# Kernel tuning notes

Hardware: AMD Instinct MI355X
Metric: run time of the kernel (lower is better)

## Reference

```python
import jax, jax.numpy as jnp
import numpy as np

B, N, C = 2, 4096, 768
H = 12  # num_heads; head_dim = C // H = 64


def setup_inputs() -> dict:
    key = jax.random.key(0)
    kx, kq, kk, kv = jax.random.split(key, 4)
    s = C ** -0.5  # keep param magnitudes sane
    return {
        "x": jax.random.normal(kx, (B, N, C), dtype=jnp.float32),
        "Wq": jax.random.normal(kq, (C, C), dtype=jnp.float32) * s,
        "Wk": jax.random.normal(kk, (C, C), dtype=jnp.float32) * s,
        "Wv": jax.random.normal(kv, (C, C), dtype=jnp.float32) * s,  # created but UNUSED, as in original
    }


def reference(x, Wq, Wk, Wv):
    b, n, c = x.shape
    hd = c // H
    # torch nn.Linear: y = x @ W.T
    q = (x @ Wq.T).reshape(b, n, H, hd).transpose(0, 2, 1, 3)  # [B,H,N,hd]
    k = (x @ Wk.T).reshape(b, n, H, hd).transpose(0, 2, 1, 3)
    # BUG preserved from source: value path uses the K projection, Wv is unused
    v = (x @ Wk.T).reshape(b, n, H, hd).transpose(0, 2, 1, 3)
    # scale by full C (not head_dim), as in source
    attn = jnp.einsum("bhqd,bhkd->bhqk", q, k) * (c ** -0.5)
    attn = jax.nn.softmax(attn, axis=-1)
    out = jnp.einsum("bhqk,bhkd->bhqd", attn, v)  # [B,H,N,hd]
    return out.transpose(0, 2, 1, 3).reshape(b, n, c)
```

## Files before the change

kernel.cpp:

```cpp
#include <hip/hip_runtime.h>

typedef __bf16 bf16;
typedef __bf16 bf16x4 __attribute__((ext_vector_type(4)));
typedef __bf16 bf16x8 __attribute__((ext_vector_type(8)));
typedef float  f32x4  __attribute__((ext_vector_type(4)));
typedef int    int4v  __attribute__((ext_vector_type(4)));

#define NTOK 4096
#define NH   12
#define HD   64
#define CDIM 768

#define K2SCALE 0.05205928442089389f

__device__ __forceinline__ bf16* swz(bf16* base, int row, int byteoff) {
  return (bf16*)((char*)base + row * 128 +
                 ((((byteoff >> 4) ^ (row & 7)) << 4) | (byteoff & 15)));
}
__device__ __forceinline__ const bf16* swz(const bf16* base, int row, int byteoff) {
  return (const bf16*)((const char*)base + row * 128 +
                 ((((byteoff >> 4) ^ (row & 7)) << 4) | (byteoff & 15)));
}

__global__ __launch_bounds__(256) void cast_kernel(
    const float* __restrict__ x, const float* __restrict__ wq, const float* __restrict__ wk,
    bf16* __restrict__ xb, bf16* __restrict__ wqb, bf16* __restrict__ wkb,
    long nx, long nw) {
  long i4 = ((long)blockIdx.x * 256 + threadIdx.x) * 4;
  if (i4 >= nx + 2 * nw) return;
  const float* src; bf16* dst;
  if (i4 < nx)            { src = x  + i4;            dst = xb  + i4; }
  else if (i4 < nx + nw)  { src = wq + (i4 - nx);     dst = wqb + (i4 - nx); }
  else                    { src = wk + (i4 - nx - nw); dst = wkb + (i4 - nx - nw); }
  f32x4 v = *(const f32x4*)src;
  *(bf16x4*)dst = __builtin_convertvector(v, bf16x4);
}

__global__ __launch_bounds__(256) void proj_kernel(
    const bf16* __restrict__ xb, const bf16* __restrict__ wqb, const bf16* __restrict__ wkb,
    bf16* __restrict__ Qb, bf16* __restrict__ Kb) {
  __shared__ __align__(16) bf16 Ap[128 * 64];
  __shared__ __align__(16) bf16 Bp[128 * 64];
  const int tid = threadIdx.x;
  const int w = tid >> 6, lane = tid & 63, l15 = lane & 15, quad = lane >> 4;
  const int m0 = blockIdx.x * 128;
  const int j0 = blockIdx.y * 128;
  const bf16* W   = blockIdx.z ? wkb : wqb;
  bf16*       Out = blockIdx.z ? Kb  : Qb;
  const float oscale = blockIdx.z ? 1.0f : K2SCALE;

  const int srow = tid >> 3, scb = (tid & 7) * 16, soff = (tid & 7) * 8;
  const bf16* pa = xb + (long)(m0 + srow) * CDIM + soff;
  const bf16* pb = W  + (long)(j0 + srow) * CDIM + soff;

  f32x4 acc[2][8] = {};
  int4v rA[4], rB[4];
#pragma unroll
  for (int i = 0; i < 4; ++i) {
    rA[i] = *(const int4v*)(pa + (long)i * 32 * CDIM);
    rB[i] = *(const int4v*)(pb + (long)i * 32 * CDIM);
  }

  for (int kt = 0; kt < CDIM / 64; ++kt) {
    __syncthreads();
#pragma unroll
    for (int i = 0; i < 4; ++i) {
      *(int4v*)swz(Ap, srow + i * 32, scb) = rA[i];
      *(int4v*)swz(Bp, srow + i * 32, scb) = rB[i];
    }
    __syncthreads();
    const long koff = (long)((kt == CDIM / 64 - 1) ? kt : kt + 1) * 64;
#pragma unroll
    for (int i = 0; i < 4; ++i) {
      rA[i] = *(const int4v*)(pa + (long)i * 32 * CDIM + koff);
      rB[i] = *(const int4v*)(pb + (long)i * 32 * CDIM + koff);
    }
#pragma unroll
    for (int kk = 0; kk < 2; ++kk) {
      bf16x8 a[2], b[8];
#pragma unroll
      for (int rt = 0; rt < 2; ++rt)
        a[rt] = *(const bf16x8*)swz(Ap, w * 32 + rt * 16 + l15, kk * 64 + quad * 16);
#pragma unroll
      for (int ct = 0; ct < 8; ++ct)
        b[ct] = *(const bf16x8*)swz(Bp, ct * 16 + l15, kk * 64 + quad * 16);
#pragma unroll
      for (int rt = 0; rt < 2; ++rt)
#pragma unroll
        for (int ct = 0; ct < 8; ++ct)
          acc[rt][ct] = __builtin_amdgcn_mfma_f32_16x16x32_bf16(a[rt], b[ct], acc[rt][ct], 0, 0, 0);
    }
  }
#pragma unroll
  for (int rt = 0; rt < 2; ++rt)
#pragma unroll
    for (int ct = 0; ct < 8; ++ct)
#pragma unroll
      for (int reg = 0; reg < 4; ++reg) {
        int m = m0 + w * 32 + rt * 16 + quad * 4 + reg;
        int j = j0 + ct * 16 + l15;
        int b = m >> 12, n = m & (NTOK - 1);
        int h = j >> 6, d = j & (HD - 1);
        Out[(((long)(b * NH + h) * NTOK + n) << 6) + d] = (bf16)(acc[rt][ct][reg] * oscale);
      }
}

__global__ __launch_bounds__(256) void transpose_kernel(
    const bf16* __restrict__ Kb, bf16* __restrict__ Ktb) {
  __shared__ __align__(16) bf16 T[64 * 72];
  const int tid = threadIdx.x;
  const int n0 = blockIdx.x * 64;
  const long bh = blockIdx.y;
#pragma unroll
  for (int i = 0; i < 2; ++i) {
    int c = tid + i * 256;
    int row = c >> 3, off = (c & 7) * 8;
    bf16x8 v = *(const bf16x8*)(Kb + ((bh << 12) + n0 + row) * HD + off);
#pragma unroll
    for (int e = 0; e < 8; ++e) T[(off + e) * 72 + row] = v[e];
  }
  __syncthreads();
#pragma unroll
  for (int i = 0; i < 2; ++i) {
    int c = tid + i * 256;
    int d = c >> 3, koff = (c & 7) * 8;
    int4v v = *(const int4v*)(&T[d * 72 + koff]);
    *(int4v*)(Ktb + ((bh << 6) + d) * (long)NTOK + n0 + koff) = v;
  }
}

__global__ __launch_bounds__(256) void attn_kernel(
    const bf16* __restrict__ Qb, const bf16* __restrict__ Kb, const bf16* __restrict__ Ktb,
    float* __restrict__ out) {
  __shared__ __align__(16) bf16 QP[128 * 64];
  __shared__ __align__(16) bf16 Ks[64 * 64];
  __shared__ __align__(16) bf16 Kts[64 * 64];

  const int tid = threadIdx.x;
  const int w = tid >> 6, lane = tid & 63, l15 = lane & 15, quad = lane >> 4;
  const int q0 = blockIdx.x * 128;
  const int bh = blockIdx.y;
  const int b = bh / NH, h = bh % NH;
  const bf16* Qhead  = Qb  + (long)bh * NTOK * HD;
  const bf16* Khead  = Kb  + (long)bh * NTOK * HD;
  const bf16* Kthead = Ktb + (long)bh * HD * NTOK;

  const int srow = tid >> 3, scb = (tid & 7) * 16, soff = (tid & 7) * 8;
  const bf16* pk  = Khead  + (long)srow * HD + soff;
  const bf16* pkt = Kthead + (long)srow * NTOK + soff;

#pragma unroll
  for (int i = 0; i < 4; ++i) {
    int c = tid + i * 256;
    int row = c >> 3, cb = (c & 7) * 16;
    int4v v = *(const int4v*)(Qhead + (long)(q0 + row) * HD + (c & 7) * 8);
    *(int4v*)swz(QP, row, cb) = v;
  }

  int4v rK[2], rKt[2];
#pragma unroll
  for (int i = 0; i < 2; ++i) {
    rK[i]  = *(const int4v*)(pk  + (long)i * 32 * HD);
    rKt[i] = *(const int4v*)(pkt + (long)i * 32 * NTOK);
  }

  __syncthreads();
  bf16x8 bq[2][2];
#pragma unroll
  for (int nt = 0; nt < 2; ++nt)
#pragma unroll
    for (int kk = 0; kk < 2; ++kk)
      bq[nt][kk] = *(const bf16x8*)swz(QP, w * 32 + nt * 16 + l15, kk * 64 + quad * 16);

  f32x4 o[4][2] = {};
  float lacc[2] = {0.f, 0.f};

  for (int kt = 0; kt < NTOK / 64; ++kt) {
    __syncthreads();
#pragma unroll
    for (int i = 0; i < 2; ++i) {
      *(int4v*)swz(Ks,  srow + i * 32, scb) = rK[i];
      *(int4v*)swz(Kts, srow + i * 32, scb) = rKt[i];
    }
    __syncthreads();

    const long knext = (long)((kt == NTOK / 64 - 1) ? kt : kt + 1) * 64;
#pragma unroll
    for (int i = 0; i < 2; ++i) {
      rK[i]  = *(const int4v*)(pk  + knext * HD + (long)i * 32 * HD);
      rKt[i] = *(const int4v*)(pkt + knext + (long)i * 32 * NTOK);
    }

    f32x4 s[4][2] = {};
#pragma unroll
    for (int kk = 0; kk < 2; ++kk) {
      bf16x8 ak[4];
#pragma unroll
      for (int mt = 0; mt < 4; ++mt)
        ak[mt] = *(const bf16x8*)swz(Ks, mt * 16 + l15, kk * 64 + quad * 16);
#pragma unroll
      for (int mt = 0; mt < 4; ++mt)
#pragma unroll
        for (int nt = 0; nt < 2; ++nt)
          s[mt][nt] = __builtin_amdgcn_mfma_f32_16x16x32_bf16(ak[mt], bq[nt][kk], s[mt][nt], 0, 0, 0);
    }

#pragma unroll
    for (int mt = 0; mt < 4; ++mt)
#pragma unroll
      for (int nt = 0; nt < 2; ++nt) {
        f32x4 p;
#pragma unroll
        for (int reg = 0; reg < 4; ++reg) p[reg] = __builtin_amdgcn_exp2f(s[mt][nt][reg]);
        lacc[nt] += (p[0] + p[1]) + (p[2] + p[3]);
        *(bf16x4*)swz(QP, w * 32 + nt * 16 + l15, mt * 32 + quad * 8) =
            __builtin_convertvector(p, bf16x4);
      }

#pragma unroll
    for (int kk = 0; kk < 2; ++kk) {
      bf16x8 av[4], bp[2];
#pragma unroll
      for (int mt = 0; mt < 4; ++mt)
        av[mt] = *(const bf16x8*)swz(Kts, mt * 16 + l15, kk * 64 + quad * 16);
#pragma unroll
      for (int nt = 0; nt < 2; ++nt)
        bp[nt] = *(const bf16x8*)swz(QP, w * 32 + nt * 16 + l15, kk * 64 + quad * 16);
#pragma unroll
      for (int mt = 0; mt < 4; ++mt)
#pragma unroll
        for (int nt = 0; nt < 2; ++nt)
          o[mt][nt] = __builtin_amdgcn_mfma_f32_16x16x32_bf16(av[mt], bp[nt], o[mt][nt], 0, 0, 0);
    }
  }

#pragma unroll
  for (int nt = 0; nt < 2; ++nt) {
    float l = lacc[nt];
    l += __shfl_xor(l, 16, 64);
    l += __shfl_xor(l, 32, 64);
    float rl = 1.0f / l;
    int n = q0 + w * 32 + nt * 16 + l15;
#pragma unroll
    for (int mt = 0; mt < 4; ++mt) {
      f32x4 v;
#pragma unroll
      for (int reg = 0; reg < 4; ++reg) v[reg] = o[mt][nt][reg] * rl;
      *(f32x4*)(&out[((long)(b * NTOK + n)) * CDIM + h * HD + mt * 16 + quad * 4]) = v;
    }
  }
}

extern "C" void kernel_launch(void* const* d_in, const int* in_sizes, int n_in,
                              void* d_out, int out_size, void* d_ws, size_t ws_size,
                              hipStream_t stream) {
  const float* x  = (const float*)d_in[0];
  const float* Wq = (const float*)d_in[1];
  const float* Wk = (const float*)d_in[2];
  float* out = (float*)d_out;
  char* ws = (char*)d_ws;

  const long NX = (long)2 * NTOK * CDIM;
  const long NW = (long)CDIM * CDIM;

  bf16* xb  = (bf16*)(ws);
  bf16* Ktb = (bf16*)(ws);
  bf16* wqb = (bf16*)(ws + NX * 2);
  bf16* wkb = (bf16*)(ws + NX * 2 + NW * 2);
  bf16* Qb  = (bf16*)(ws + NX * 2 + NW * 4);
  bf16* Kb  = (bf16*)(ws + NX * 2 + NW * 4 + NX * 2);

  long tot4 = (NX + 2 * NW) / 4;
  cast_kernel<<<dim3((tot4 + 255) / 256), 256, 0, stream>>>(x, Wq, Wk, xb, wqb, wkb, NX, NW);
  proj_kernel<<<dim3(8192 / 128, CDIM / 128, 2), 256, 0, stream>>>(xb, wqb, wkb, Qb, Kb);
  transpose_kernel<<<dim3(NTOK / 64, 2 * NH), 256, 0, stream>>>(Kb, Ktb);
  attn_kernel<<<dim3(NTOK / 128, 2 * NH), 256, 0, stream>>>(Qb, Kb, Ktb, out);
}
```

Measured before the change: 237.2 us.

## Split attention key range across two blocks and add combine kernel

Adds a grid z-dimension that splits the key loop into halves, with each block writing unnormalized partial outputs and row sums to workspace. A new combine kernel sums the partials and normalizes into the final output. This raises parallelism and shortens each block's serial loop, at the cost of extra global traffic for the partial buffers and one more launch. It falls back to the single-pass path when the workspace is too small.

```diff
diff --git a/kernel.cpp b/kernel.cpp
--- a/kernel.cpp
+++ b/kernel.cpp
@@ -131,7 +131,8 @@
 
 __global__ __launch_bounds__(256) void attn_kernel(
     const bf16* __restrict__ Qb, const bf16* __restrict__ Kb, const bf16* __restrict__ Ktb,
-    float* __restrict__ out) {
+    float* __restrict__ out, float* __restrict__ Opart, float* __restrict__ lpart,
+    int nsplit) {
   __shared__ __align__(16) bf16 QP[128 * 64];
   __shared__ __align__(16) bf16 Ks[64 * 64];
   __shared__ __align__(16) bf16 Kts[64 * 64];
@@ -140,7 +141,10 @@
   const int w = tid >> 6, lane = tid & 63, l15 = lane & 15, quad = lane >> 4;
   const int q0 = blockIdx.x * 128;
   const int bh = blockIdx.y;
+  const int half = blockIdx.z;
   const int b = bh / NH, h = bh % NH;
+  const int ktiles = (NTOK / 64) / nsplit;
+  const int kt0 = half * ktiles, kt1 = kt0 + ktiles;
   const bf16* Qhead  = Qb  + (long)bh * NTOK * HD;
   const bf16* Khead  = Kb  + (long)bh * NTOK * HD;
   const bf16* Kthead = Ktb + (long)bh * HD * NTOK;
@@ -160,8 +164,8 @@
   int4v rK[2], rKt[2];
 #pragma unroll
   for (int i = 0; i < 2; ++i) {
-    rK[i]  = *(const int4v*)(pk  + (long)i * 32 * HD);
-    rKt[i] = *(const int4v*)(pkt + (long)i * 32 * NTOK);
+    rK[i]  = *(const int4v*)(pk  + (long)kt0 * 64 * HD + (long)i * 32 * HD);
+    rKt[i] = *(const int4v*)(pkt + (long)kt0 * 64 + (long)i * 32 * NTOK);
   }
 
   __syncthreads();
@@ -175,7 +179,7 @@
   f32x4 o[4][2] = {};
   float lacc[2] = {0.f, 0.f};
 
-  for (int kt = 0; kt < NTOK / 64; ++kt) {
+  for (int kt = kt0; kt < kt1; ++kt) {
     __syncthreads();
 #pragma unroll
     for (int i = 0; i < 2; ++i) {
@@ -184,7 +188,7 @@
     }
     __syncthreads();
 
-    const long knext = (long)((kt == NTOK / 64 - 1) ? kt : kt + 1) * 64;
+    const long knext = (long)((kt == kt1 - 1) ? kt : kt + 1) * 64;
 #pragma unroll
     for (int i = 0; i < 2; ++i) {
       rK[i]  = *(const int4v*)(pk  + knext * HD + (long)i * 32 * HD);
@@ -234,21 +238,55 @@
     }
   }
 
-#pragma unroll
-  for (int nt = 0; nt < 2; ++nt) {
-    float l = lacc[nt];
-    l += __shfl_xor(l, 16, 64);
-    l += __shfl_xor(l, 32, 64);
-    float rl = 1.0f / l;
-    int n = q0 + w * 32 + nt * 16 + l15;
-#pragma unroll
-    for (int mt = 0; mt < 4; ++mt) {
-      f32x4 v;
-#pragma unroll
-      for (int reg = 0; reg < 4; ++reg) v[reg] = o[mt][nt][reg] * rl;
-      *(f32x4*)(&out[((long)(b * NTOK + n)) * CDIM + h * HD + mt * 16 + quad * 4]) = v;
-    }
-  }
+  if (nsplit == 1) {
+#pragma unroll
+    for (int nt = 0; nt < 2; ++nt) {
+      float l = lacc[nt];
+      l += __shfl_xor(l, 16, 64);
+      l += __shfl_xor(l, 32, 64);
+      float rl = 1.0f / l;
+      int n = q0 + w * 32 + nt * 16 + l15;
+#pragma unroll
+      for (int mt = 0; mt < 4; ++mt) {
+        f32x4 v;
+#pragma unroll
+        for (int reg = 0; reg < 4; ++reg) v[reg] = o[mt][nt][reg] * rl;
+        *(f32x4*)(&out[((long)(b * NTOK + n)) * CDIM + h * HD + mt * 16 + quad * 4]) = v;
+      }
+    }
+  } else {
+    const long rbase = ((long)(half * 2 * NH + bh)) << 12;
+#pragma unroll
+    for (int nt = 0; nt < 2; ++nt) {
+      float l = lacc[nt];
+      l += __shfl_xor(l, 16, 64);
+      l += __shfl_xor(l, 32, 64);
+      int n = q0 + w * 32 + nt * 16 + l15;
+      if (quad == 0) lpart[rbase + n] = l;
+#pragma unroll
+      for (int mt = 0; mt < 4; ++mt)
+        *(f32x4*)(&Opart[((rbase + n) << 6) + mt * 16 + quad * 4]) = o[mt][nt];
+    }
+  }
+}
+
+__global__ __launch_bounds__(256) void combine_kernel(
+    const float* __restrict__ Opart, const float* __restrict__ lpart,
+    float* __restrict__ out) {
+  const int t = threadIdx.x;
+  const long r = (long)blockIdx.x * 16 + (t >> 4);
+  const int d = (t & 15) * 4;
+  const long RS = (long)2 * NH * NTOK;
+  f32x4 a = *(const f32x4*)(Opart + (r << 6) + d);
+  f32x4 c = *(const f32x4*)(Opart + ((RS + r) << 6) + d);
+  float l = lpart[r] + lpart[RS + r];
+  float rl = 1.0f / l;
+  int bh = (int)(r >> 12), n = (int)(r & (NTOK - 1));
+  int b = bh / NH, h = bh % NH;
+  f32x4 v;
+#pragma unroll
+  for (int e = 0; e < 4; ++e) v[e] = (a[e] + c[e]) * rl;
+  *(f32x4*)(&out[((long)(b * NTOK + n)) * CDIM + h * HD + d]) = v;
 }
 
 extern "C" void kernel_launch(void* const* d_in, const int* in_sizes, int n_in,
@@ -269,10 +307,20 @@
   bf16* wkb = (bf16*)(ws + NX * 2 + NW * 2);
   bf16* Qb  = (bf16*)(ws + NX * 2 + NW * 4);
   bf16* Kb  = (bf16*)(ws + NX * 2 + NW * 4 + NX * 2);
+  const size_t base = (size_t)(NX * 6 + NW * 4);
+
+  const long ROWS = (long)2 * NH * NTOK;
+  float* Opart = (float*)(ws + base);
+  float* lpart = (float*)(ws + base + (size_t)2 * ROWS * HD * 4);
+  const size_t need = base + (size_t)2 * ROWS * HD * 4 + (size_t)2 * ROWS * 4;
+  const int nsplit = (ws_size >= need) ? 2 : 1;
 
   long tot4 = (NX + 2 * NW) / 4;
   cast_kernel<<<dim3((tot4 + 255) / 256), 256, 0, stream>>>(x, Wq, Wk, xb, wqb, wkb, NX, NW);
   proj_kernel<<<dim3(8192 / 128, CDIM / 128, 2), 256, 0, stream>>>(xb, wqb, wkb, Qb, Kb);
   transpose_kernel<<<dim3(NTOK / 64, 2 * NH), 256, 0, stream>>>(Kb, Ktb);
-  attn_kernel<<<dim3(NTOK / 128, 2 * NH), 256, 0, stream>>>(Qb, Kb, Ktb, out);
-}
+  attn_kernel<<<dim3(NTOK / 128, 2 * NH, nsplit), 256, 0, stream>>>(
+      Qb, Kb, Ktb, out, Opart, lpart, nsplit);
+  if (nsplit == 2)
+    combine_kernel<<<dim3(ROWS / 16), 256, 0, stream>>>(Opart, lpart, out);
+}
```

New measurement: 252.6 us. 1.06x slower.

## Split attention warps 2x2 over query and key halves with LDS reduction

Applied to the files above, without the earlier changes.

Reassigns the four waves of the attention block from a 4-way query split into a 2x2 split over query halves (64 rows) and key halves (32 keys) of each tile. Each wave now loads fewer K fragments per QK^T step and does a single PV k-step, which cuts redundant LDS reads of K and Kt. The cost is a larger output accumulator per wave (4x4 tiles instead of 4x2, more registers) and an end-of-kernel cross-wave reduction of partial outputs and row sums through shared memory.

```diff
diff --git a/kernel.cpp b/kernel.cpp
--- a/kernel.cpp
+++ b/kernel.cpp
@@ -132,12 +132,15 @@
 __global__ __launch_bounds__(256) void attn_kernel(
     const bf16* __restrict__ Qb, const bf16* __restrict__ Kb, const bf16* __restrict__ Ktb,
     float* __restrict__ out) {
-  __shared__ __align__(16) bf16 QP[128 * 64];
-  __shared__ __align__(16) bf16 Ks[64 * 64];
-  __shared__ __align__(16) bf16 Kts[64 * 64];
+  __shared__ __align__(16) bf16 SH[128 * 64 + 64 * 64 + 64 * 64 + 1024];
+  bf16* QP  = SH;
+  bf16* Ks  = SH + 128 * 64;
+  bf16* Kts = SH + 128 * 64 + 64 * 64;
+  float* lbuf = (float*)(SH + 128 * 64 + 2 * 64 * 64);
 
   const int tid = threadIdx.x;
   const int w = tid >> 6, lane = tid & 63, l15 = lane & 15, quad = lane >> 4;
+  const int qhalf = w >> 1, khalf = w & 1;
   const int q0 = blockIdx.x * 128;
   const int bh = blockIdx.y;
   const int b = bh / NH, h = bh % NH;
@@ -165,15 +168,15 @@
   }
 
   __syncthreads();
-  bf16x8 bq[2][2];
-#pragma unroll
-  for (int nt = 0; nt < 2; ++nt)
+  bf16x8 bq[4][2];
+#pragma unroll
+  for (int nt = 0; nt < 4; ++nt)
 #pragma unroll
     for (int kk = 0; kk < 2; ++kk)
-      bq[nt][kk] = *(const bf16x8*)swz(QP, w * 32 + nt * 16 + l15, kk * 64 + quad * 16);
-
-  f32x4 o[4][2] = {};
-  float lacc[2] = {0.f, 0.f};
+      bq[nt][kk] = *(const bf16x8*)swz(QP, qhalf * 64 + nt * 16 + l15, kk * 64 + quad * 16);
+
+  f32x4 o[4][4] = {};
+  float lacc[4] = {0.f, 0.f, 0.f, 0.f};
 
   for (int kt = 0; kt < NTOK / 64; ++kt) {
     __syncthreads();
@@ -191,62 +194,82 @@
       rKt[i] = *(const int4v*)(pkt + knext + (long)i * 32 * NTOK);
     }
 
-    f32x4 s[4][2] = {};
+    f32x4 s[2][4] = {};
 #pragma unroll
     for (int kk = 0; kk < 2; ++kk) {
-      bf16x8 ak[4];
-#pragma unroll
-      for (int mt = 0; mt < 4; ++mt)
-        ak[mt] = *(const bf16x8*)swz(Ks, mt * 16 + l15, kk * 64 + quad * 16);
-#pragma unroll
-      for (int mt = 0; mt < 4; ++mt)
-#pragma unroll
-        for (int nt = 0; nt < 2; ++nt)
+      bf16x8 ak[2];
+#pragma unroll
+      for (int mt = 0; mt < 2; ++mt)
+        ak[mt] = *(const bf16x8*)swz(Ks, khalf * 32 + mt * 16 + l15, kk * 64 + quad * 16);
+#pragma unroll
+      for (int mt = 0; mt < 2; ++mt)
+#pragma unroll
+        for (int nt = 0; nt < 4; ++nt)
           s[mt][nt] = __builtin_amdgcn_mfma_f32_16x16x32_bf16(ak[mt], bq[nt][kk], s[mt][nt], 0, 0, 0);
     }
 
 #pragma unroll
-    for (int mt = 0; mt < 4; ++mt)
-#pragma unroll
-      for (int nt = 0; nt < 2; ++nt) {
+    for (int mt = 0; mt < 2; ++mt)
+#pragma unroll
+      for (int nt = 0; nt < 4; ++nt) {
         f32x4 p;
 #pragma unroll
         for (int reg = 0; reg < 4; ++reg) p[reg] = __builtin_amdgcn_exp2f(s[mt][nt][reg]);
         lacc[nt] += (p[0] + p[1]) + (p[2] + p[3]);
-        *(bf16x4*)swz(QP, w * 32 + nt * 16 + l15, mt * 32 + quad * 8) =
+        *(bf16x4*)swz(QP, qhalf * 64 + nt * 16 + l15, khalf * 64 + mt * 32 + quad * 8) =
             __builtin_convertvector(p, bf16x4);
       }
 
-#pragma unroll
-    for (int kk = 0; kk < 2; ++kk) {
-      bf16x8 av[4], bp[2];
-#pragma unroll
-      for (int mt = 0; mt < 4; ++mt)
-        av[mt] = *(const bf16x8*)swz(Kts, mt * 16 + l15, kk * 64 + quad * 16);
-#pragma unroll
-      for (int nt = 0; nt < 2; ++nt)
-        bp[nt] = *(const bf16x8*)swz(QP, w * 32 + nt * 16 + l15, kk * 64 + quad * 16);
-#pragma unroll
-      for (int mt = 0; mt < 4; ++mt)
-#pragma unroll
-        for (int nt = 0; nt < 2; ++nt)
-          o[mt][nt] = __builtin_amdgcn_mfma_f32_16x16x32_bf16(av[mt], bp[nt], o[mt][nt], 0, 0, 0);
-    }
-  }
-
-#pragma unroll
-  for (int nt = 0; nt < 2; ++nt) {
+    bf16x8 av[4], bp[4];
+#pragma unroll
+    for (int mt = 0; mt < 4; ++mt)
+      av[mt] = *(const bf16x8*)swz(Kts, mt * 16 + l15, khalf * 64 + quad * 16);
+#pragma unroll
+    for (int nt = 0; nt < 4; ++nt)
+      bp[nt] = *(const bf16x8*)swz(QP, qhalf * 64 + nt * 16 + l15, khalf * 64 + quad * 16);
+#pragma unroll
+    for (int mt = 0; mt < 4; ++mt)
+#pragma unroll
+      for (int nt = 0; nt < 4; ++nt)
+        o[mt][nt] = __builtin_amdgcn_mfma_f32_16x16x32_bf16(av[mt], bp[nt], o[mt][nt], 0, 0, 0);
+  }
+
+  float lq[4];
+#pragma unroll
+  for (int nt = 0; nt < 4; ++nt) {
     float l = lacc[nt];
     l += __shfl_xor(l, 16, 64);
     l += __shfl_xor(l, 32, 64);
-    float rl = 1.0f / l;
-    int n = q0 + w * 32 + nt * 16 + l15;
-#pragma unroll
-    for (int mt = 0; mt < 4; ++mt) {
-      f32x4 v;
-#pragma unroll
-      for (int reg = 0; reg < 4; ++reg) v[reg] = o[mt][nt][reg] * rl;
-      *(f32x4*)(&out[((long)(b * NTOK + n)) * CDIM + h * HD + mt * 16 + quad * 4]) = v;
+    lq[nt] = l;
+  }
+  __syncthreads();
+  float* sc = qhalf ? (float*)Ks : (float*)QP;
+  if (khalf == 1) {
+#pragma unroll
+    for (int mt = 0; mt < 4; ++mt)
+#pragma unroll
+      for (int nt = 0; nt < 4; ++nt)
+        *(f32x4*)(sc + ((mt * 4 + nt) * 64 + lane) * 4) = o[mt][nt];
+#pragma unroll
+    for (int nt = 0; nt < 4; ++nt) lbuf[qhalf * 256 + nt * 64 + lane] = lq[nt];
+  }
+  __syncthreads();
+  if (khalf == 0) {
+    float rl[4];
+#pragma unroll
+    for (int nt = 0; nt < 4; ++nt)
+      rl[nt] = 1.0f / (lq[nt] + lbuf[qhalf * 256 + nt * 64 + lane]);
+#pragma unroll
+    for (int nt = 0; nt < 4; ++nt) {
+      int n = q0 + qhalf * 64 + nt * 16 + l15;
+#pragma unroll
+      for (int mt = 0; mt < 4; ++mt) {
+        f32x4 po = *(const f32x4*)(sc + ((mt * 4 + nt) * 64 + lane) * 4);
+        f32x4 v;
+#pragma unroll
+        for (int reg = 0; reg < 4; ++reg) v[reg] = (o[mt][nt][reg] + po[reg]) * rl[nt];
+        *(f32x4*)(&out[((long)(b * NTOK + n)) * CDIM + h * HD + mt * 16 + quad * 4]) = v;
+      }
     }
   }
 }
```

Result: slower. 250.0 us (+5.4%).

## Use single-wave attention blocks that load K tiles straight from global memory

Applied to the files above, without the earlier changes.

The attention kernel changes from 256-thread blocks sharing K/Kt tiles in LDS to 64-thread single-wave blocks. Each wave reads K and K-transposed fragments directly from global memory into registers, and only the P tile stays in LDS. The grid is reordered so heads vary fastest, which lets concurrent blocks of the same query range share K through L2. This removes the __syncthreads barriers and the LDS staging, but K traffic to L1/L2 rises fourfold and there is no explicit prefetch of the next tile.

```diff
diff --git a/kernel.cpp b/kernel.cpp
--- a/kernel.cpp
+++ b/kernel.cpp
@@ -129,81 +129,50 @@
   }
 }
 
-__global__ __launch_bounds__(256) void attn_kernel(
+__global__ __launch_bounds__(64, 3) void attn_kernel(
     const bf16* __restrict__ Qb, const bf16* __restrict__ Kb, const bf16* __restrict__ Ktb,
     float* __restrict__ out) {
-  __shared__ __align__(16) bf16 QP[128 * 64];
-  __shared__ __align__(16) bf16 Ks[64 * 64];
-  __shared__ __align__(16) bf16 Kts[64 * 64];
-
-  const int tid = threadIdx.x;
-  const int w = tid >> 6, lane = tid & 63, l15 = lane & 15, quad = lane >> 4;
-  const int q0 = blockIdx.x * 128;
-  const int bh = blockIdx.y;
+  __shared__ __align__(16) bf16 P[32 * 64];
+
+  const int lane = threadIdx.x;
+  const int l15 = lane & 15, quad = lane >> 4;
+  const int bh = blockIdx.x;
+  const int q0 = blockIdx.y * 32;
   const int b = bh / NH, h = bh % NH;
   const bf16* Qhead  = Qb  + (long)bh * NTOK * HD;
   const bf16* Khead  = Kb  + (long)bh * NTOK * HD;
   const bf16* Kthead = Ktb + (long)bh * HD * NTOK;
 
-  const int srow = tid >> 3, scb = (tid & 7) * 16, soff = (tid & 7) * 8;
-  const bf16* pk  = Khead  + (long)srow * HD + soff;
-  const bf16* pkt = Kthead + (long)srow * NTOK + soff;
-
-#pragma unroll
-  for (int i = 0; i < 4; ++i) {
-    int c = tid + i * 256;
-    int row = c >> 3, cb = (c & 7) * 16;
-    int4v v = *(const int4v*)(Qhead + (long)(q0 + row) * HD + (c & 7) * 8);
-    *(int4v*)swz(QP, row, cb) = v;
-  }
-
-  int4v rK[2], rKt[2];
-#pragma unroll
-  for (int i = 0; i < 2; ++i) {
-    rK[i]  = *(const int4v*)(pk  + (long)i * 32 * HD);
-    rKt[i] = *(const int4v*)(pkt + (long)i * 32 * NTOK);
-  }
-
-  __syncthreads();
   bf16x8 bq[2][2];
 #pragma unroll
   for (int nt = 0; nt < 2; ++nt)
 #pragma unroll
     for (int kk = 0; kk < 2; ++kk)
-      bq[nt][kk] = *(const bf16x8*)swz(QP, w * 32 + nt * 16 + l15, kk * 64 + quad * 16);
+      bq[nt][kk] = *(const bf16x8*)(Qhead + (long)(q0 + nt * 16 + l15) * HD + kk * 32 + quad * 8);
 
   f32x4 o[4][2] = {};
   float lacc[2] = {0.f, 0.f};
 
   for (int kt = 0; kt < NTOK / 64; ++kt) {
-    __syncthreads();
-#pragma unroll
-    for (int i = 0; i < 2; ++i) {
-      *(int4v*)swz(Ks,  srow + i * 32, scb) = rK[i];
-      *(int4v*)swz(Kts, srow + i * 32, scb) = rKt[i];
-    }
-    __syncthreads();
-
-    const long knext = (long)((kt == NTOK / 64 - 1) ? kt : kt + 1) * 64;
-#pragma unroll
-    for (int i = 0; i < 2; ++i) {
-      rK[i]  = *(const int4v*)(pk  + knext * HD + (long)i * 32 * HD);
-      rKt[i] = *(const int4v*)(pkt + knext + (long)i * 32 * NTOK);
-    }
+    const long k0 = (long)kt * 64;
+
+    bf16x8 ak[4][2], av[4][2];
+#pragma unroll
+    for (int mt = 0; mt < 4; ++mt)
+#pragma unroll
+      for (int kk = 0; kk < 2; ++kk) {
+        ak[mt][kk] = *(const bf16x8*)(Khead + (k0 + mt * 16 + l15) * HD + kk * 32 + quad * 8);
+        av[mt][kk] = *(const bf16x8*)(Kthead + (long)(mt * 16 + l15) * NTOK + k0 + kk * 32 + quad * 8);
+      }
 
     f32x4 s[4][2] = {};
 #pragma unroll
-    for (int kk = 0; kk < 2; ++kk) {
-      bf16x8 ak[4];
+    for (int kk = 0; kk < 2; ++kk)
 #pragma unroll
       for (int mt = 0; mt < 4; ++mt)
-        ak[mt] = *(const bf16x8*)swz(Ks, mt * 16 + l15, kk * 64 + quad * 16);
-#pragma unroll
-      for (int mt = 0; mt < 4; ++mt)
 #pragma unroll
         for (int nt = 0; nt < 2; ++nt)
-          s[mt][nt] = __builtin_amdgcn_mfma_f32_16x16x32_bf16(ak[mt], bq[nt][kk], s[mt][nt], 0, 0, 0);
-    }
+          s[mt][nt] = __builtin_amdgcn_mfma_f32_16x16x32_bf16(ak[mt][kk], bq[nt][kk], s[mt][nt], 0, 0, 0);
 
 #pragma unroll
     for (int mt = 0; mt < 4; ++mt)
@@ -213,24 +182,21 @@
 #pragma unroll
         for (int reg = 0; reg < 4; ++reg) p[reg] = __builtin_amdgcn_exp2f(s[mt][nt][reg]);
         lacc[nt] += (p[0] + p[1]) + (p[2] + p[3]);
-        *(bf16x4*)swz(QP, w * 32 + nt * 16 + l15, mt * 32 + quad * 8) =
+        *(bf16x4*)swz(P, nt * 16 + l15, mt * 32 + quad * 8) =
             __builtin_convertvector(p, bf16x4);
       }
 
 #pragma unroll
     for (int kk = 0; kk < 2; ++kk) {
-      bf16x8 av[4], bp[2];
+      bf16x8 bp[2];
+#pragma unroll
+      for (int nt = 0; nt < 2; ++nt)
+        bp[nt] = *(const bf16x8*)swz(P, nt * 16 + l15, kk * 64 + quad * 16);
 #pragma unroll
       for (int mt = 0; mt < 4; ++mt)
-        av[mt] = *(const bf16x8*)swz(Kts, mt * 16 + l15, kk * 64 + quad * 16);
-#pragma unroll
-      for (int nt = 0; nt < 2; ++nt)
-        bp[nt] = *(const bf16x8*)swz(QP, w * 32 + nt * 16 + l15, kk * 64 + quad * 16);
-#pragma unroll
-      for (int mt = 0; mt < 4; ++mt)
 #pragma unroll
         for (int nt = 0; nt < 2; ++nt)
-          o[mt][nt] = __builtin_amdgcn_mfma_f32_16x16x32_bf16(av[mt], bp[nt], o[mt][nt], 0, 0, 0);
+          o[mt][nt] = __builtin_amdgcn_mfma_f32_16x16x32_bf16(av[mt][kk], bp[nt], o[mt][nt], 0, 0, 0);
     }
   }
 
@@ -240,7 +206,7 @@
     l += __shfl_xor(l, 16, 64);
     l += __shfl_xor(l, 32, 64);
     float rl = 1.0f / l;
-    int n = q0 + w * 32 + nt * 16 + l15;
+    int n = q0 + nt * 16 + l15;
 #pragma unroll
     for (int mt = 0; mt < 4; ++mt) {
       f32x4 v;
@@ -274,5 +240,5 @@
   cast_kernel<<<dim3((tot4 + 255) / 256), 256, 0, stream>>>(x, Wq, Wk, xb, wqb, wkb, NX, NW);
   proj_kernel<<<dim3(8192 / 128, CDIM / 128, 2), 256, 0, stream>>>(xb, wqb, wkb, Qb, Kb);
   transpose_kernel<<<dim3(NTOK / 64, 2 * NH), 256, 0, stream>>>(Kb, Ktb);
-  attn_kernel<<<dim3(NTOK / 128, 2 * NH), 256, 0, stream>>>(Qb, Kb, Ktb, out);
-}
+  attn_kernel<<<dim3(2 * NH, NTOK / 32), 64, 0, stream>>>(Qb, Kb, Ktb, out);
+}
```

New measurement: 452.8 us. 90.9% more time.
